# Kernel optimization log

Hardware: AMD Instinct MI355X
Metric: run time of the kernel (lower is better)

The kernel has to match this reference:

```python
import jax, jax.numpy as jnp
import numpy as np

H = 256
B = 32768
ADV, GOOD, BOX, RAMP = 8, 8, 16, 8
OTHER = ADV + GOOD - 1
OBS = 10 + 10 * OTHER + 13 * BOX + 12 * RAMP  # 464


def _lin(k, din, dout):
    return jax.random.normal(k, (din, dout), dtype=jnp.float32) * (1.0 / np.sqrt(din))


def setup_inputs() -> dict:
    key = jax.random.key(0)
    ks = jax.random.split(key, 12)
    return {
        "inputs": jax.random.normal(ks[0], (B, OBS), dtype=jnp.float32),
        "W_self": _lin(ks[1], 10, H), "b_self": jnp.zeros((H,), jnp.float32),
        "W_other": _lin(ks[2], 10, H), "b_other": jnp.zeros((H,), jnp.float32),
        "W_box": _lin(ks[3], 13, H), "b_box": jnp.zeros((H,), jnp.float32),
        "W_ramp": _lin(ks[4], 12, H), "b_ramp": jnp.zeros((H,), jnp.float32),
        "corr_other": _lin(ks[5], H, H),
        "corr_box": _lin(ks[6], H, H),
        "corr_ramp": _lin(ks[7], H, H),
        "W_fc": _lin(ks[8], H, H), "b_fc": jnp.zeros((H,), jnp.float32),
        "W_e1": _lin(ks[9], 4 * H, H), "b_e1": jnp.zeros((H,), jnp.float32),
        "W_e2": _lin(ks[10], H, H), "b_e2": jnp.zeros((H,), jnp.float32),
        "adv_num": ADV, "good_num": GOOD, "box_num": BOX, "ramp_num": RAMP,
        "agent_i": 0,
    }


def _attend_pool(emb_self, corr, ents, W, b):
    # ents: [B, N, F] raw entity features -> encode, bilinear score vs self, softmax, pool
    emb = jnp.tanh(jnp.einsum('bnf,fh->bnh', ents, W) + b)        # [B,N,H]
    beta = jnp.einsum('bh,hk,bnk->bn', emb_self, corr, emb)        # [B,N]
    alpha = jax.nn.softmax(beta, axis=1)                           # [B,N]
    return jnp.einsum('bn,bnh->bh', alpha, emb)                    # [B,H]


def reference(inputs, W_self, b_self, W_other, b_other, W_box, b_box,
              W_ramp, b_ramp, corr_other, corr_box, corr_ramp,
              W_fc, b_fc, W_e1, b_e1, W_e2, b_e2,
              adv_num, good_num, box_num, ramp_num, agent_i):
    bsz = inputs.shape[0]
    other_nums = adv_num + good_num - 1
    o0 = 10
    o1 = o0 + 10 * other_nums
    o2 = o1 + 13 * box_num
    o3 = o2 + 12 * ramp_num

    self_in = inputs[:, :o0]                                   # [B,10]
    other_in = inputs[:, o0:o1].reshape(bsz, other_nums, 10)   # [B,N_o,10]
    box_in = inputs[:, o1:o2].reshape(bsz, box_num, 13)        # [B,N_b,13]
    ramp_in = inputs[:, o2:o3].reshape(bsz, ramp_num, 12)      # [B,N_r,12]

    emb_self = jnp.tanh(self_in @ W_self + b_self)             # [B,H]

    vi_other = _attend_pool(emb_self, corr_other, other_in, W_other, b_other)
    vi_box = _attend_pool(emb_self, corr_box, box_in, W_box, b_box)
    vi_ramp = _attend_pool(emb_self, corr_ramp, ramp_in, W_ramp, b_ramp)

    gi = jnp.tanh(emb_self @ W_fc + b_fc)                      # [B,H]
    cat = jnp.concatenate([gi, vi_other, vi_box, vi_ramp], axis=1)  # [B,4H]
    h = jnp.tanh(cat @ W_e1 + b_e1)
    return jnp.tanh(h @ W_e2 + b_e2)                           # [B,H]
```

## Files before the change

### kernel.cpp

```cpp
#include <hip/hip_runtime.h>
#include <hip/hip_bf16.h>

#define HDIM   256
#define OBS    464
#define MROWS  16

#define OFF_FC 196608
#define OFF_E1 262144
#define OFF_E2 524288
#define TOTW   589824

typedef __attribute__((ext_vector_type(8))) short short8;
typedef __attribute__((ext_vector_type(4))) float f32x4;
typedef unsigned short u16;

__device__ __forceinline__ float fast_tanh(float x) {
    float e = __expf(2.0f * x);
    return 1.0f - 2.0f * __builtin_amdgcn_rcpf(e + 1.0f);
}

template <bool BF16>
__device__ __forceinline__ float loadf(const void* p, int i) {
    if constexpr (BF16)
        return __bfloat162float(((const __hip_bfloat16*)p)[i]);
    else
        return ((const float*)p)[i];
}

__device__ __forceinline__ u16 f2bf(float x) {
    __hip_bfloat16 b = __float2bfloat16(x);
    return *reinterpret_cast<u16*>(&b);
}

__device__ __forceinline__ float b2f(u16 u) {
    return __uint_as_float(((unsigned)u) << 16);
}

__device__ __forceinline__ void split1(float v, u16& hi, u16& lo) {
    unsigned u = __float_as_uint(v);
    hi = (u16)(u >> 16);
    lo = f2bf(v - __uint_as_float(u & 0xffff0000u));
}

__device__ __forceinline__ f32x4 mfma3(short8 ah, short8 al, short8 bh, short8 bl, f32x4 c) {
    c = __builtin_amdgcn_mfma_f32_16x16x32_bf16(ah, bh, c, 0, 0, 0);
    c = __builtin_amdgcn_mfma_f32_16x16x32_bf16(al, bh, c, 0, 0, 0);
    c = __builtin_amdgcn_mfma_f32_16x16x32_bf16(ah, bl, c, 0, 0, 0);
    return c;
}

__device__ __forceinline__ int pidx(int row, int col) {
    return row * HDIM + (col ^ ((row & 7) << 3));
}

__device__ __forceinline__ void store_act(u16* __restrict__ hiP, u16* __restrict__ loP,
                                          int row, int col, float v) {
    u16 h, s;
    split1(v, h, s);
    const int i = pidx(row, col);
    hiP[i] = h;
    loP[i] = s;
}

__device__ __forceinline__ void lda_p(const u16* __restrict__ hiP, const u16* __restrict__ loP,
                                      int l, int kbase, short8& ah, short8& al) {
    const int row = l & 15;
    const int col = kbase + ((l >> 4) << 3);
    const int idx = row * HDIM + (col ^ ((row & 7) << 3));
    ah = *(const short8*)(hiP + idx);
    al = *(const short8*)(loP + idx);
}

__device__ __forceinline__ void mm4(const u16* __restrict__ hiP, const u16* __restrict__ loP,
                                    const u16* __restrict__ Whi, const u16* __restrict__ Wlo,
                                    int seg, int ks0, int wv, int l, f32x4 acc[4]) {
#pragma unroll 2
    for (int ks = 0; ks < 8; ++ks) {
        short8 ah, al;
        lda_p(hiP, loP, l, ks << 5, ah, al);
        const u16* bp = Whi + seg + ((ks0 + ks) << 13) + (l << 3);
        const u16* lp = Wlo + seg + ((ks0 + ks) << 13) + (l << 3);
#pragma unroll
        for (int c4 = 0; c4 < 4; ++c4) {
            const int ct = (wv << 2) + c4;
            short8 bh = *(const short8*)(bp + (ct << 9));
            short8 bl = *(const short8*)(lp + (ct << 9));
            acc[c4] = mfma3(ah, al, bh, bl, acc[c4]);
        }
    }
}

template <bool BF16, int N, int F, int BASE>
__device__ __forceinline__ void attend_group(int wv, int l, const void* __restrict__ x,
                                             int rb, int Bn,
                                             u16* __restrict__ hiP, u16* __restrict__ loP,
                                             const void* __restrict__ W,
                                             const void* __restrict__ b) {
    float wreg[F][4];
#pragma unroll
    for (int k = 0; k < F; ++k)
#pragma unroll
        for (int c = 0; c < 4; ++c)
            wreg[k][c] = loadf<BF16>(W, k * HDIM + c * 64 + l);
    const float b0 = loadf<BF16>(b, l);
    const float b1 = loadf<BF16>(b, 64 + l);
    const float b2 = loadf<BF16>(b, 128 + l);
    const float b3 = loadf<BF16>(b, 192 + l);
#pragma unroll 1
    for (int t = 0; t < 4; ++t) {
        const int r = (wv << 2) + t;
        int row = rb + r; if (row >= Bn) row = Bn - 1;
        const unsigned urow = (unsigned)__builtin_amdgcn_readfirstlane(row);
        const unsigned* xd = (const unsigned*)x + ((urow * OBS + BASE) >> 1);
        const float*    xf = (const float*)x + (urow * OBS + BASE);
        const int i0 = pidx(r, l), i1 = pidx(r, 64 + l), i2 = pidx(r, 128 + l), i3 = pidx(r, 192 + l);
        const float q0 = b2f(hiP[i0]) + b2f(loP[i0]);
        const float q1 = b2f(hiP[i1]) + b2f(loP[i1]);
        const float q2 = b2f(hiP[i2]) + b2f(loP[i2]);
        const float q3 = b2f(hiP[i3]) + b2f(loP[i3]);
        float s = 0.0f;
        float v0 = 0.f, v1 = 0.f, v2 = 0.f, v3 = 0.f;
#pragma unroll 4
        for (int n = 0; n < N; ++n) {
            float a0 = b0, a1 = b1, a2 = b2, a3 = b3;
#pragma unroll
            for (int k = 0; k < F; ++k) {
                const int jj = n * F + k;
                float xv;
                if constexpr (BF16) {
                    unsigned d = xd[jj >> 1];
                    xv = __uint_as_float((jj & 1) ? (d & 0xffff0000u) : (d << 16));
                } else {
                    xv = xf[jj];
                }
                a0 = fmaf(xv, wreg[k][0], a0);
                a1 = fmaf(xv, wreg[k][1], a1);
                a2 = fmaf(xv, wreg[k][2], a2);
                a3 = fmaf(xv, wreg[k][3], a3);
            }
            float e0 = fast_tanh(a0), e1 = fast_tanh(a1);
            float e2 = fast_tanh(a2), e3 = fast_tanh(a3);
            float p = q0 * e0;
            p = fmaf(q1, e1, p);
            p = fmaf(q2, e2, p);
            p = fmaf(q3, e3, p);
#pragma unroll
            for (int mm = 1; mm < 64; mm <<= 1) p += __shfl_xor(p, mm, 64);
            float w = __expf(p);
            s += w;
            v0 = fmaf(w, e0, v0);
            v1 = fmaf(w, e1, v1);
            v2 = fmaf(w, e2, v2);
            v3 = fmaf(w, e3, v3);
        }
        float inv = __builtin_amdgcn_rcpf(s);
        store_act(hiP, loP, r, l,       v0 * inv);
        store_act(hiP, loP, r, 64 + l,  v1 * inv);
        store_act(hiP, loP, r, 128 + l, v2 * inv);
        store_act(hiP, loP, r, 192 + l, v3 * inv);
    }
}

__global__ void dtype_probe(const unsigned short* __restrict__ x, int* __restrict__ flag) {
    if (threadIdx.x == 0 && blockIdx.x == 0) {
        int cnt = 0;
        for (int i = 0; i < 256; ++i) {
            unsigned short u = x[2 * i];
            int e = (u >> 7) & 0xFF;
            if (e >= 118 && e <= 132) cnt++;
        }
        *flag = (cnt >= 128) ? 1 : 0;
    }
}

template <bool BF16>
__global__ void prep_weights(const void* __restrict__ c0, const void* __restrict__ c1,
                             const void* __restrict__ c2, const void* __restrict__ fc,
                             const void* __restrict__ e1, const void* __restrict__ e2,
                             u16* __restrict__ Whi, u16* __restrict__ Wlo,
                             const int* __restrict__ flag) {
    if (*flag != (BF16 ? 1 : 0)) return;
    int idx = blockIdx.x * 256 + threadIdx.x;
    if (idx >= TOTW) return;
    const void* src;
    int base;
    if (idx < OFF_FC)      { int m = idx >> 16; src = (m == 0) ? c0 : ((m == 1) ? c1 : c2); base = m << 16; }
    else if (idx < OFF_E1) { src = fc; base = OFF_FC; }
    else if (idx < OFF_E2) { src = e1; base = OFF_E1; }
    else                   { src = e2; base = OFF_E2; }
    int local = idx - base;
    int i  = local & 7;
    int ln = (local >> 3) & 63;
    int ct = (local >> 9) & 15;
    int ks = local >> 13;
    int k = (ks << 5) + ((ln >> 4) << 3) + i;
    int c = (ct << 4) + (ln & 15);
    float v = loadf<BF16>(src, k * HDIM + c);
    u16 h, s;
    split1(v, h, s);
    Whi[idx] = h;
    Wlo[idx] = s;
}

template <bool BF16>
__global__ __launch_bounds__(256, 2) void obs_mfma(
    const void* __restrict__ inputs,
    const void* __restrict__ W_self, const void* __restrict__ b_self,
    const void* __restrict__ W_other, const void* __restrict__ b_other,
    const void* __restrict__ W_box, const void* __restrict__ b_box,
    const void* __restrict__ W_ramp, const void* __restrict__ b_ramp,
    const void* __restrict__ b_fc, const void* __restrict__ b_e1,
    const void* __restrict__ b_e2,
    const u16* __restrict__ Whi, const u16* __restrict__ Wlo,
    void* __restrict__ out, const int* __restrict__ flag, int Bn) {
    if (*flag != (BF16 ? 1 : 0)) return;

    __shared__ u16 sAh[MROWS * HDIM], sAl[MROWS * HDIM];
    __shared__ u16 sBh[MROWS * HDIM], sBl[MROWS * HDIM];
    __shared__ float sC[16 * 256];

    const int tid = threadIdx.x;
    const int rb = blockIdx.x * MROWS;
    const int wv = tid >> 6, l = tid & 63;
    const f32x4 z = {0.f, 0.f, 0.f, 0.f};

    {
        float acc[MROWS];
        float bv = loadf<BF16>(b_self, tid);
#pragma unroll
        for (int r = 0; r < MROWS; ++r) acc[r] = bv;
#pragma unroll
        for (int k = 0; k < 10; ++k) {
            float w = loadf<BF16>(W_self, k * HDIM + tid);
#pragma unroll
            for (int r = 0; r < MROWS; ++r) {
                int row = rb + r; if (row >= Bn) row = Bn - 1;
                acc[r] = fmaf(loadf<BF16>(inputs, row * OBS + k), w, acc[r]);
            }
        }
#pragma unroll
        for (int r = 0; r < MROWS; ++r)
            store_act(sAh, sAl, r, tid, fast_tanh(acc[r]));
    }
    __syncthreads();

    {
        f32x4 acc[4] = {z, z, z, z};
        mm4(sAh, sAl, Whi, Wlo, OFF_FC, 0, wv, l, acc);
#pragma unroll
        for (int c4 = 0; c4 < 4; ++c4) {
            const int ct = (wv << 2) + c4, col = (ct << 4) + (l & 15);
            float bv = loadf<BF16>(b_fc, col);
#pragma unroll
            for (int i = 0; i < 4; ++i) {
                const int row = ((l >> 4) << 2) + i;
                store_act(sBh, sBl, row, col, fast_tanh(acc[c4][i] + bv));
            }
        }
    }
    __syncthreads();

    {
        f32x4 acc[4] = {z, z, z, z};
        mm4(sBh, sBl, Whi, Wlo, OFF_E1, 0, wv, l, acc);
#pragma unroll
        for (int c4 = 0; c4 < 4; ++c4)
#pragma unroll
            for (int i = 0; i < 4; ++i)
                sC[(c4 * 4 + i) * 256 + tid] = acc[c4][i];
    }
    __syncthreads();

#pragma unroll
    for (int g = 0; g < 3; ++g) {
        {
            f32x4 acc[4] = {z, z, z, z};
            mm4(sAh, sAl, Whi, Wlo, g << 16, 0, wv, l, acc);
#pragma unroll
            for (int c4 = 0; c4 < 4; ++c4) {
                const int ct = (wv << 2) + c4, col = (ct << 4) + (l & 15);
#pragma unroll
                for (int i = 0; i < 4; ++i) {
                    const int row = ((l >> 4) << 2) + i;
                    store_act(sBh, sBl, row, col, acc[c4][i]);
                }
            }
        }
        __syncthreads();
        if (g == 0)      attend_group<BF16, 15, 10,  10>(wv, l, inputs, rb, Bn, sBh, sBl, W_other, b_other);
        else if (g == 1) attend_group<BF16, 16, 13, 160>(wv, l, inputs, rb, Bn, sBh, sBl, W_box,  b_box);
        else             attend_group<BF16,  8, 12, 368>(wv, l, inputs, rb, Bn, sBh, sBl, W_ramp, b_ramp);
        __syncthreads();
        {
            f32x4 acc[4];
#pragma unroll
            for (int c4 = 0; c4 < 4; ++c4)
#pragma unroll
                for (int i = 0; i < 4; ++i)
                    acc[c4][i] = sC[(c4 * 4 + i) * 256 + tid];
            mm4(sBh, sBl, Whi, Wlo, OFF_E1, (g + 1) << 3, wv, l, acc);
#pragma unroll
            for (int c4 = 0; c4 < 4; ++c4)
#pragma unroll
                for (int i = 0; i < 4; ++i)
                    sC[(c4 * 4 + i) * 256 + tid] = acc[c4][i];
        }
        __syncthreads();
    }

#pragma unroll
    for (int c4 = 0; c4 < 4; ++c4) {
        const int ct = (wv << 2) + c4, col = (ct << 4) + (l & 15);
        float bv = loadf<BF16>(b_e1, col);
#pragma unroll
        for (int i = 0; i < 4; ++i) {
            const int row = ((l >> 4) << 2) + i;
            store_act(sAh, sAl, row, col, fast_tanh(sC[(c4 * 4 + i) * 256 + tid] + bv));
        }
    }
    __syncthreads();

    {
        f32x4 acc[4] = {z, z, z, z};
        mm4(sAh, sAl, Whi, Wlo, OFF_E2, 0, wv, l, acc);
#pragma unroll
        for (int c4 = 0; c4 < 4; ++c4) {
            const int ct = (wv << 2) + c4, col = (ct << 4) + (l & 15);
            float bv = loadf<BF16>(b_e2, col);
#pragma unroll
            for (int i = 0; i < 4; ++i) {
                const int row = rb + ((l >> 4) << 2) + i;
                if (row < Bn) {
                    float v = fast_tanh(acc[c4][i] + bv);
                    if constexpr (BF16)
                        ((__hip_bfloat16*)out)[row * HDIM + col] = __float2bfloat16(v);
                    else
                        ((float*)out)[row * HDIM + col] = v;
                }
            }
        }
    }
}

extern "C" void kernel_launch(void* const* d_in, const int* in_sizes, int n_in,
                              void* d_out, int out_size, void* d_ws, size_t ws_size,
                              hipStream_t stream) {
    const int Bn = in_sizes[0] / OBS;
    int* flag = (int*)d_ws;
    u16* Whi = (u16*)((char*)d_ws + 256);
    u16* Wlo = Whi + TOTW;

    dtype_probe<<<1, 64, 0, stream>>>((const unsigned short*)d_in[0], flag);

    const int pgrid = (TOTW + 255) / 256;
    prep_weights<true><<<pgrid, 256, 0, stream>>>(
        d_in[9], d_in[10], d_in[11], d_in[12], d_in[14], d_in[16], Whi, Wlo, flag);
    prep_weights<false><<<pgrid, 256, 0, stream>>>(
        d_in[9], d_in[10], d_in[11], d_in[12], d_in[14], d_in[16], Whi, Wlo, flag);

    const int grid = (Bn + MROWS - 1) / MROWS;
    obs_mfma<true><<<grid, 256, 0, stream>>>(
        d_in[0], d_in[1], d_in[2], d_in[3], d_in[4], d_in[5], d_in[6], d_in[7],
        d_in[8], d_in[13], d_in[15], d_in[17], Whi, Wlo, d_out, flag, Bn);
    obs_mfma<false><<<grid, 256, 0, stream>>>(
        d_in[0], d_in[1], d_in[2], d_in[3], d_in[4], d_in[5], d_in[6], d_in[7],
        d_in[8], d_in[13], d_in[15], d_in[17], Whi, Wlo, d_out, flag, Bn);
}
```

Baseline: 571.9 us.

## Split each 16-row tile across eight waves instead of four

```diff
diff --git a/kernel.cpp b/kernel.cpp
--- a/kernel.cpp
+++ b/kernel.cpp
@@ -4,6 +4,7 @@
 #define HDIM   256
 #define OBS    464
 #define MROWS  16
+#define NW     8
 
 #define OFF_FC 196608
 #define OFF_E1 262144
@@ -71,9 +72,9 @@
     al = *(const short8*)(loP + idx);
 }
 
-__device__ __forceinline__ void mm4(const u16* __restrict__ hiP, const u16* __restrict__ loP,
+__device__ __forceinline__ void mm2(const u16* __restrict__ hiP, const u16* __restrict__ loP,
                                     const u16* __restrict__ Whi, const u16* __restrict__ Wlo,
-                                    int seg, int ks0, int wv, int l, f32x4 acc[4]) {
+                                    int seg, int ks0, int wv, int l, f32x4 acc[2]) {
 #pragma unroll 2
     for (int ks = 0; ks < 8; ++ks) {
         short8 ah, al;
@@ -81,8 +82,8 @@
         const u16* bp = Whi + seg + ((ks0 + ks) << 13) + (l << 3);
         const u16* lp = Wlo + seg + ((ks0 + ks) << 13) + (l << 3);
 #pragma unroll
-        for (int c4 = 0; c4 < 4; ++c4) {
-            const int ct = (wv << 2) + c4;
+        for (int c4 = 0; c4 < 2; ++c4) {
+            const int ct = (wv << 1) + c4;
             short8 bh = *(const short8*)(bp + (ct << 9));
             short8 bl = *(const short8*)(lp + (ct << 9));
             acc[c4] = mfma3(ah, al, bh, bl, acc[c4]);
@@ -107,8 +108,8 @@
     const float b2 = loadf<BF16>(b, 128 + l);
     const float b3 = loadf<BF16>(b, 192 + l);
 #pragma unroll 1
-    for (int t = 0; t < 4; ++t) {
-        const int r = (wv << 2) + t;
+    for (int t = 0; t < 2; ++t) {
+        const int r = (wv << 1) + t;
         int row = rb + r; if (row >= Bn) row = Bn - 1;
         const unsigned urow = (unsigned)__builtin_amdgcn_readfirstlane(row);
         const unsigned* xd = (const unsigned*)x + ((urow * OBS + BASE) >> 1);
@@ -203,7 +204,7 @@
 }
 
 template <bool BF16>
-__global__ __launch_bounds__(256, 2) void obs_mfma(
+__global__ __launch_bounds__(512, 4) void obs_mfma(
     const void* __restrict__ inputs,
     const void* __restrict__ W_self, const void* __restrict__ b_self,
     const void* __restrict__ W_other, const void* __restrict__ b_other,
@@ -217,7 +218,7 @@
 
     __shared__ u16 sAh[MROWS * HDIM], sAl[MROWS * HDIM];
     __shared__ u16 sBh[MROWS * HDIM], sBl[MROWS * HDIM];
-    __shared__ float sC[16 * 256];
+    __shared__ float sC[8 * 512];
 
     const int tid = threadIdx.x;
     const int rb = blockIdx.x * MROWS;
@@ -225,31 +226,32 @@
     const f32x4 z = {0.f, 0.f, 0.f, 0.f};
 
     {
-        float acc[MROWS];
-        float bv = loadf<BF16>(b_self, tid);
-#pragma unroll
-        for (int r = 0; r < MROWS; ++r) acc[r] = bv;
+        const int col = tid & 255, rh = tid >> 8;
+        float acc[8];
+        float bv = loadf<BF16>(b_self, col);
+#pragma unroll
+        for (int r = 0; r < 8; ++r) acc[r] = bv;
 #pragma unroll
         for (int k = 0; k < 10; ++k) {
-            float w = loadf<BF16>(W_self, k * HDIM + tid);
-#pragma unroll
-            for (int r = 0; r < MROWS; ++r) {
-                int row = rb + r; if (row >= Bn) row = Bn - 1;
+            float w = loadf<BF16>(W_self, k * HDIM + col);
+#pragma unroll
+            for (int r = 0; r < 8; ++r) {
+                int row = rb + rh * 8 + r; if (row >= Bn) row = Bn - 1;
                 acc[r] = fmaf(loadf<BF16>(inputs, row * OBS + k), w, acc[r]);
             }
         }
 #pragma unroll
-        for (int r = 0; r < MROWS; ++r)
-            store_act(sAh, sAl, r, tid, fast_tanh(acc[r]));
+        for (int r = 0; r < 8; ++r)
+            store_act(sAh, sAl, rh * 8 + r, col, fast_tanh(acc[r]));
     }
     __syncthreads();
 
     {
-        f32x4 acc[4] = {z, z, z, z};
-        mm4(sAh, sAl, Whi, Wlo, OFF_FC, 0, wv, l, acc);
-#pragma unroll
-        for (int c4 = 0; c4 < 4; ++c4) {
-            const int ct = (wv << 2) + c4, col = (ct << 4) + (l & 15);
+        f32x4 acc[2] = {z, z};
+        mm2(sAh, sAl, Whi, Wlo, OFF_FC, 0, wv, l, acc);
+#pragma unroll
+        for (int c4 = 0; c4 < 2; ++c4) {
+            const int ct = (wv << 1) + c4, col = (ct << 4) + (l & 15);
             float bv = loadf<BF16>(b_fc, col);
 #pragma unroll
             for (int i = 0; i < 4; ++i) {
@@ -261,24 +263,24 @@
     __syncthreads();
 
     {
-        f32x4 acc[4] = {z, z, z, z};
-        mm4(sBh, sBl, Whi, Wlo, OFF_E1, 0, wv, l, acc);
-#pragma unroll
-        for (int c4 = 0; c4 < 4; ++c4)
+        f32x4 acc[2] = {z, z};
+        mm2(sBh, sBl, Whi, Wlo, OFF_E1, 0, wv, l, acc);
+#pragma unroll
+        for (int c4 = 0; c4 < 2; ++c4)
 #pragma unroll
             for (int i = 0; i < 4; ++i)
-                sC[(c4 * 4 + i) * 256 + tid] = acc[c4][i];
+                sC[(c4 * 4 + i) * 512 + tid] = acc[c4][i];
     }
     __syncthreads();
 
 #pragma unroll
     for (int g = 0; g < 3; ++g) {
         {
-            f32x4 acc[4] = {z, z, z, z};
-            mm4(sAh, sAl, Whi, Wlo, g << 16, 0, wv, l, acc);
-#pragma unroll
-            for (int c4 = 0; c4 < 4; ++c4) {
-                const int ct = (wv << 2) + c4, col = (ct << 4) + (l & 15);
+            f32x4 acc[2] = {z, z};
+            mm2(sAh, sAl, Whi, Wlo, g << 16, 0, wv, l, acc);
+#pragma unroll
+            for (int c4 = 0; c4 < 2; ++c4) {
+                const int ct = (wv << 1) + c4, col = (ct << 4) + (l & 15);
 #pragma unroll
                 for (int i = 0; i < 4; ++i) {
                     const int row = ((l >> 4) << 2) + i;
@@ -292,40 +294,40 @@
         else             attend_group<BF16,  8, 12, 368>(wv, l, inputs, rb, Bn, sBh, sBl, W_ramp, b_ramp);
         __syncthreads();
         {
-            f32x4 acc[4];
-#pragma unroll
-            for (int c4 = 0; c4 < 4; ++c4)
+            f32x4 acc[2];
+#pragma unroll
+            for (int c4 = 0; c4 < 2; ++c4)
 #pragma unroll
                 for (int i = 0; i < 4; ++i)
-                    acc[c4][i] = sC[(c4 * 4 + i) * 256 + tid];
-            mm4(sBh, sBl, Whi, Wlo, OFF_E1, (g + 1) << 3, wv, l, acc);
-#pragma unroll
-            for (int c4 = 0; c4 < 4; ++c4)
+                    acc[c4][i] = sC[(c4 * 4 + i) * 512 + tid];
+            mm2(sBh, sBl, Whi, Wlo, OFF_E1, (g + 1) << 3, wv, l, acc);
+#pragma unroll
+            for (int c4 = 0; c4 < 2; ++c4)
 #pragma unroll
                 for (int i = 0; i < 4; ++i)
-                    sC[(c4 * 4 + i) * 256 + tid] = acc[c4][i];
+                    sC[(c4 * 4 + i) * 512 + tid] = acc[c4][i];
         }
         __syncthreads();
     }
 
 #pragma unroll
-    for (int c4 = 0; c4 < 4; ++c4) {
-        const int ct = (wv << 2) + c4, col = (ct << 4) + (l & 15);
+    for (int c4 = 0; c4 < 2; ++c4) {
+        const int ct = (wv << 1) + c4, col = (ct << 4) + (l & 15);
         float bv = loadf<BF16>(b_e1, col);
 #pragma unroll
         for (int i = 0; i < 4; ++i) {
             const int row = ((l >> 4) << 2) + i;
-            store_act(sAh, sAl, row, col, fast_tanh(sC[(c4 * 4 + i) * 256 + tid] + bv));
+            store_act(sAh, sAl, row, col, fast_tanh(sC[(c4 * 4 + i) * 512 + tid] + bv));
         }
     }
     __syncthreads();
 
     {
-        f32x4 acc[4] = {z, z, z, z};
-        mm4(sAh, sAl, Whi, Wlo, OFF_E2, 0, wv, l, acc);
-#pragma unroll
-        for (int c4 = 0; c4 < 4; ++c4) {
-            const int ct = (wv << 2) + c4, col = (ct << 4) + (l & 15);
+        f32x4 acc[2] = {z, z};
+        mm2(sAh, sAl, Whi, Wlo, OFF_E2, 0, wv, l, acc);
+#pragma unroll
+        for (int c4 = 0; c4 < 2; ++c4) {
+            const int ct = (wv << 1) + c4, col = (ct << 4) + (l & 15);
             float bv = loadf<BF16>(b_e2, col);
 #pragma unroll
             for (int i = 0; i < 4; ++i) {
@@ -359,10 +361,10 @@
         d_in[9], d_in[10], d_in[11], d_in[12], d_in[14], d_in[16], Whi, Wlo, flag);
 
     const int grid = (Bn + MROWS - 1) / MROWS;
-    obs_mfma<true><<<grid, 256, 0, stream>>>(
+    obs_mfma<true><<<grid, 512, 0, stream>>>(
         d_in[0], d_in[1], d_in[2], d_in[3], d_in[4], d_in[5], d_in[6], d_in[7],
         d_in[8], d_in[13], d_in[15], d_in[17], Whi, Wlo, d_out, flag, Bn);
-    obs_mfma<false><<<grid, 256, 0, stream>>>(
+    obs_mfma<false><<<grid, 512, 0, stream>>>(
         d_in[0], d_in[1], d_in[2], d_in[3], d_in[4], d_in[5], d_in[6], d_in[7],
         d_in[8], d_in[13], d_in[15], d_in[17], Whi, Wlo, d_out, flag, Bn);
 }
```

Measured after the change: 526.8 us. -7.9%, faster.
